# Kernel tuning notes

Hardware: AMD Instinct MI355X
Metric: run time of the kernel (lower is better)

Reference implementation:

```python
import jax, jax.numpy as jnp
import numpy as np

N_A = 50000
N_B = 50000
E = 1600000
D_IN = 128
HID = 128
OUT = 64
NUM_LAYERS = 2


def setup_inputs() -> dict:
    key = jax.random.key(0)
    ks = jax.random.split(key, 16)
    s = 0.05  # weight scale
    return {
        "x_a": jax.random.normal(ks[0], (N_A, D_IN), jnp.float32),
        "x_b": jax.random.normal(ks[1], (N_B, D_IN), jnp.float32),
        "ei_ab": jax.random.randint(ks[2], (2, E), 0, N_A, jnp.int32),  # row0: src in a, row1: dst in b
        "ei_ba": jax.random.randint(ks[3], (2, E), 0, N_B, jnp.int32),
        "Wa_in": jax.random.normal(ks[4], (D_IN, HID), jnp.float32) * s,
        "ba_in": jnp.zeros((HID,), jnp.float32),
        "Wb_in": jax.random.normal(ks[5], (D_IN, HID), jnp.float32) * s,
        "bb_in": jnp.zeros((HID,), jnp.float32),
        "Wl_ab": jax.random.normal(ks[6], (NUM_LAYERS, HID, HID), jnp.float32) * s,
        "Wr_ab": jax.random.normal(ks[7], (NUM_LAYERS, HID, HID), jnp.float32) * s,
        "bl_ab": jnp.zeros((NUM_LAYERS, HID), jnp.float32),
        "Wl_ba": jax.random.normal(ks[8], (NUM_LAYERS, HID, HID), jnp.float32) * s,
        "Wr_ba": jax.random.normal(ks[9], (NUM_LAYERS, HID, HID), jnp.float32) * s,
        "bl_ba": jnp.zeros((NUM_LAYERS, HID), jnp.float32),
        "W_out": jax.random.normal(ks[10], (HID, OUT), jnp.float32) * s,
        "b_out": jnp.zeros((OUT,), jnp.float32),
    }


def _sage_mean(x_src, src_idx, dst_idx, n_dst):
    # mean aggregation of neighbor features onto destination nodes
    msgs = x_src[src_idx]                                   # [E, H] gather
    summed = jax.ops.segment_sum(msgs, dst_idx, num_segments=n_dst)  # [N_dst, H]
    cnt = jax.ops.segment_sum(jnp.ones((src_idx.shape[0],), x_src.dtype), dst_idx, num_segments=n_dst)
    return summed / jnp.maximum(cnt, 1.0)[:, None]


def reference(x_a, x_b, ei_ab, ei_ba, Wa_in, ba_in, Wb_in, bb_in,
              Wl_ab, Wr_ab, bl_ab, Wl_ba, Wr_ba, bl_ba, W_out, b_out):
    # per-node-type input projection + relu
    h_a = jax.nn.relu(x_a @ Wa_in + ba_in)
    h_b = jax.nn.relu(x_b @ Wb_in + bb_in)
    for l in range(NUM_LAYERS):
        # edge type (a -> b): SAGEConv -> new b features
        mean_b = _sage_mean(h_a, ei_ab[0], ei_ab[1], N_B)
        out_b = mean_b @ Wl_ab[l] + bl_ab[l] + h_b @ Wr_ab[l]
        # edge type (b -> a): SAGEConv -> new a features
        mean_a = _sage_mean(h_b, ei_ba[0], ei_ba[1], N_A)
        out_a = mean_a @ Wl_ba[l] + bl_ba[l] + h_a @ Wr_ba[l]
        # HeteroConv aggr='sum': single conv per dst type here; then relu
        h_a = jax.nn.relu(out_a)
        h_b = jax.nn.relu(out_b)
    return h_a @ W_out + b_out
```

## Files before the change

### kernel.cpp

```cpp
#include <hip/hip_runtime.h>

#define N_A   50000
#define N_B   50000
#define NE    1600000
#define HID   128
#define DOUT  64

#define BSH    6
#define BNODES 64
#define NBKT   782
#define ACH    16384

__global__ __launch_bounds__(256)
void bucket_hist(const int* __restrict__ dst, int* __restrict__ cnt, int n) {
    __shared__ int h[NBKT];
    for (int i = threadIdx.x; i < NBKT; i += 256) h[i] = 0;
    __syncthreads();
    for (int i = blockIdx.x * 256 + threadIdx.x; i < n; i += gridDim.x * 256)
        atomicAdd(&h[dst[i] >> BSH], 1);
    __syncthreads();
    for (int i = threadIdx.x; i < NBKT; i += 256)
        if (h[i]) atomicAdd(&cnt[i], h[i]);
}

__global__ __launch_bounds__(1024)
void bucket_scan(const int* __restrict__ cnt, int* __restrict__ base,
                 int* __restrict__ gcur, int etot) {
    __shared__ int s[1024];
    const int g = blockIdx.x;
    cnt  += g * NBKT;
    base += g * (NBKT + 1);
    gcur += g * NBKT;
    int t = threadIdx.x;
    int v = (t < NBKT) ? cnt[t] : 0;
    s[t] = v;
    __syncthreads();
    for (int off = 1; off < 1024; off <<= 1) {
        int x = (t >= off) ? s[t - off] : 0;
        __syncthreads();
        s[t] += x;
        __syncthreads();
    }
    if (t < NBKT) { int b = s[t] - v; base[t] = b; gcur[t] = b; }
    if (t == NBKT) base[t] = etot;
}

__global__ __launch_bounds__(256)
void bucket_scatter(const int* __restrict__ src, const int* __restrict__ dst,
                    int* __restrict__ gcur, unsigned int* __restrict__ ebuf, int n) {
    __shared__ int hist[NBKT];
    __shared__ int lbase[NBKT];
    for (int i = threadIdx.x; i < NBKT; i += 256) hist[i] = 0;
    __syncthreads();
    const int c0 = blockIdx.x * ACH;
    const int c1 = min(c0 + ACH, n);
    for (int i = c0 + threadIdx.x; i < c1; i += 256)
        atomicAdd(&hist[dst[i] >> BSH], 1);
    __syncthreads();
    for (int i = threadIdx.x; i < NBKT; i += 256) {
        int h = hist[i];
        lbase[i] = h ? atomicAdd(&gcur[i], h) : 0;
    }
    __syncthreads();
    for (int i = threadIdx.x; i < NBKT; i += 256) hist[i] = 0;
    __syncthreads();
    for (int i = c0 + threadIdx.x; i < c1; i += 256) {
        int d = dst[i], sv = src[i];
        int b = d >> BSH;
        int p = lbase[b] + atomicAdd(&hist[b], 1);
        ebuf[p] = ((unsigned)(d & (BNODES - 1)) << 16) | (unsigned)sv;
    }
}

__global__ __launch_bounds__(256)
void bucket_csr(const unsigned int* __restrict__ ebuf, const int* __restrict__ base,
                int* __restrict__ indptr, int* __restrict__ col, int nnodes) {
    __shared__ int hist[BNODES];
    __shared__ int lbase[BNODES];
    __shared__ int cur[BNODES];
    const int t = threadIdx.x;
    const int b = blockIdx.x;
    const int e0 = base[b], e1 = base[b + 1];
    if (t < BNODES) { hist[t] = 0; cur[t] = 0; }
    __syncthreads();
    for (int i = e0 + t; i < e1; i += 256)
        atomicAdd(&hist[ebuf[i] >> 16], 1);
    __syncthreads();
    if (t == 0) {
        int acc = 0;
        for (int j = 0; j < BNODES; ++j) { lbase[j] = acc; acc += hist[j]; }
    }
    __syncthreads();
    {
        int node = (b << BSH) + t;
        if (t < BNODES && node <= nnodes) indptr[node] = e0 + lbase[t];
        if (t == BNODES && node - 1 < nnodes && node - 1 == nnodes - 1 && b == NBKT - 1)
            ;
    }
    if (t < BNODES) {
        int node = (b << BSH) + t;
        if (node == nnodes) indptr[node] = e0 + lbase[t];
    }
    if (b == NBKT - 1 && t == 0 && (NBKT << BSH) == nnodes) indptr[nnodes] = e1;
    for (int i = e0 + t; i < e1; i += 256) {
        unsigned pe = ebuf[i];
        int dl = pe >> 16;
        int p = e0 + lbase[dl] + atomicAdd(&cur[dl], 1);
        col[p] = (int)(pe & 0xffffu);
    }
}

__global__ __launch_bounds__(256)
void agg_mean(const float* __restrict__ h, const int* __restrict__ indptr,
              const int* __restrict__ col, float* __restrict__ outm, int n) {
    int w = threadIdx.x >> 6;
    int l = threadIdx.x & 63;
    int v = blockIdx.x * 4 + w;
    if (v >= n) return;
    int s = indptr[v], e = indptr[v + 1];
    const int half = l >> 5;
    const int q    = l & 31;
    const float4* h4 = (const float4*)h;
    float ax = 0.f, ay = 0.f, az = 0.f, aw = 0.f;
    int i = s;
    for (; i + 4 <= e; i += 4) {
        int u0 = col[i + half];
        int u1 = col[i + 2 + half];
        float4 x0 = h4[u0 * 32 + q];
        float4 x1 = h4[u1 * 32 + q];
        ax += x0.x + x1.x; ay += x0.y + x1.y;
        az += x0.z + x1.z; aw += x0.w + x1.w;
    }
    for (; i + 2 <= e; i += 2) {
        int u = col[i + half];
        float4 x = h4[u * 32 + q];
        ax += x.x; ay += x.y; az += x.z; aw += x.w;
    }
    if (i < e && half == 0) {
        float4 x = h4[col[i] * 32 + q];
        ax += x.x; ay += x.y; az += x.z; aw += x.w;
    }
    ax += __shfl_xor(ax, 32);
    ay += __shfl_xor(ay, 32);
    az += __shfl_xor(az, 32);
    aw += __shfl_xor(aw, 32);
    if (half == 0) {
        float inv = 1.0f / fmaxf((float)(e - s), 1.0f);
        float4 o;
        o.x = ax * inv; o.y = ay * inv; o.z = az * inv; o.w = aw * inv;
        ((float4*)outm)[v * 32 + q] = o;
    }
}

#define AS 132

__device__ __forceinline__ void fma4(float4& a, float s, const float4& w) {
    a.x += s * w.x; a.y += s * w.y; a.z += s * w.z; a.w += s * w.w;
}

template <int COLS, bool TWO, bool RELU>
__global__ __launch_bounds__(256)
void gemm_rt(const float* __restrict__ A, const float* __restrict__ B,
             const float* __restrict__ W1, const float* __restrict__ W2,
             const float* __restrict__ bias, float* __restrict__ out, int nrows) {
    constexpr int NCH = COLS / 64;
    __shared__ float Asm[64 * AS];
    __shared__ float Wsm[128 * 64];
    const int t = threadIdx.x;
    const int p = t >> 4, m = t & 15, m4 = m * 4;
    const int r0 = 4 * p;
    const int rbase = blockIdx.x * 64;

    float4 acc[NCH][4];
#pragma unroll
    for (int c = 0; c < NCH; ++c)
#pragma unroll
        for (int i = 0; i < 4; ++i)
            acc[c][i] = make_float4(0.f, 0.f, 0.f, 0.f);

#pragma unroll
    for (int sidx = 0; sidx < (TWO ? 2 : 1); ++sidx) {
        const float* Asrc = (TWO && sidx) ? B : A;
        const float* Wsrc = (TWO && sidx) ? W2 : W1;
        __syncthreads();
        {
            const float4* g = (const float4*)Asrc;
#pragma unroll
            for (int it = 0; it < 8; ++it) {
                int f = t + 256 * it;
                int r = f >> 5, c = f & 31;
                int gr = rbase + r;
                float4 v = make_float4(0.f, 0.f, 0.f, 0.f);
                if (gr < nrows) v = g[(size_t)gr * 32 + c];
                *(float4*)&Asm[r * AS + 4 * c] = v;
            }
        }
#pragma unroll
        for (int ch = 0; ch < NCH; ++ch) {
            if (ch > 0) __syncthreads();
            {
                const float4* gw = (const float4*)Wsrc;
#pragma unroll
                for (int it = 0; it < 8; ++it) {
                    int f = t + 256 * it;
                    int k = f >> 4, c4 = f & 15;
                    float4 v = gw[k * (COLS / 4) + ch * 16 + c4];
                    *(float4*)&Wsm[k * 64 + 4 * c4] = v;
                }
            }
            __syncthreads();
#pragma unroll 2
            for (int k = 0; k < 128; k += 4) {
                float4 w0 = *(const float4*)&Wsm[(k + 0) * 64 + m4];
                float4 w1 = *(const float4*)&Wsm[(k + 1) * 64 + m4];
                float4 w2 = *(const float4*)&Wsm[(k + 2) * 64 + m4];
                float4 w3 = *(const float4*)&Wsm[(k + 3) * 64 + m4];
#pragma unroll
                for (int i = 0; i < 4; ++i) {
                    float4 a = *(const float4*)&Asm[(r0 + i) * AS + k];
                    fma4(acc[ch][i], a.x, w0);
                    fma4(acc[ch][i], a.y, w1);
                    fma4(acc[ch][i], a.z, w2);
                    fma4(acc[ch][i], a.w, w3);
                }
            }
        }
    }

#pragma unroll
    for (int ch = 0; ch < NCH; ++ch) {
        float4 b4 = *(const float4*)&bias[ch * 64 + m4];
#pragma unroll
        for (int i = 0; i < 4; ++i) {
            int r = rbase + r0 + i;
            if (r < nrows) {
                float4 v = acc[ch][i];
                v.x += b4.x; v.y += b4.y; v.z += b4.z; v.w += b4.w;
                if (RELU) {
                    v.x = fmaxf(v.x, 0.f); v.y = fmaxf(v.y, 0.f);
                    v.z = fmaxf(v.z, 0.f); v.w = fmaxf(v.w, 0.f);
                }
                *(float4*)&out[(size_t)r * COLS + ch * 64 + m4] = v;
            }
        }
    }
}

extern "C" void kernel_launch(void* const* d_in, const int* in_sizes, int n_in,
                              void* d_out, int out_size, void* d_ws, size_t ws_size,
                              hipStream_t stream) {
    const float* x_a   = (const float*)d_in[0];
    const float* x_b   = (const float*)d_in[1];
    const int*   ei_ab = (const int*)d_in[2];
    const int*   ei_ba = (const int*)d_in[3];
    const float* Wa_in = (const float*)d_in[4];
    const float* ba_in = (const float*)d_in[5];
    const float* Wb_in = (const float*)d_in[6];
    const float* bb_in = (const float*)d_in[7];
    const float* Wl_ab = (const float*)d_in[8];
    const float* Wr_ab = (const float*)d_in[9];
    const float* bl_ab = (const float*)d_in[10];
    const float* Wl_ba = (const float*)d_in[11];
    const float* Wr_ba = (const float*)d_in[12];
    const float* bl_ba = (const float*)d_in[13];
    const float* W_out = (const float*)d_in[14];
    const float* b_out = (const float*)d_in[15];
    float* out = (float*)d_out;

    char* w = (char*)d_ws;
    auto alloc = [&](size_t bytes) -> void* {
        void* pp = (void*)w;
        w += (bytes + 255) & ~(size_t)255;
        return pp;
    };
    float* hA0 = (float*)alloc((size_t)N_A * HID * 4);
    float* hA1 = (float*)alloc((size_t)N_A * HID * 4);
    float* hB0 = (float*)alloc((size_t)N_B * HID * 4);
    float* hB1 = (float*)alloc((size_t)N_B * HID * 4);
    unsigned int* ebuf_ab = (unsigned int*)alloc((size_t)NE * 4);
    unsigned int* ebuf_ba = (unsigned int*)alloc((size_t)NE * 4);
    int* col_ab   = (int*)alloc((size_t)NE * 4);
    int* col_ba   = (int*)alloc((size_t)NE * 4);
    int* indptr_b = (int*)alloc((size_t)(N_B + 1) * 4);
    int* indptr_a = (int*)alloc((size_t)(N_A + 1) * 4);
    int* cnt  = (int*)alloc((size_t)2 * NBKT * 4);
    int* base = (int*)alloc((size_t)2 * (NBKT + 1) * 4);
    int* gcur = (int*)alloc((size_t)2 * NBKT * 4);

    hipMemsetAsync(cnt, 0, (size_t)2 * NBKT * 4, stream);
    bucket_hist<<<256, 256, 0, stream>>>(ei_ab + NE, cnt, NE);
    bucket_hist<<<256, 256, 0, stream>>>(ei_ba + NE, cnt + NBKT, NE);
    bucket_scan<<<2, 1024, 0, stream>>>(cnt, base, gcur, NE);
    const int scat_blocks = (NE + ACH - 1) / ACH;
    bucket_scatter<<<scat_blocks, 256, 0, stream>>>(ei_ab, ei_ab + NE, gcur, ebuf_ab, NE);
    bucket_scatter<<<scat_blocks, 256, 0, stream>>>(ei_ba, ei_ba + NE, gcur + NBKT, ebuf_ba, NE);
    const int* base_ab = base;
    const int* base_ba = base + (NBKT + 1);
    bucket_csr<<<NBKT, 256, 0, stream>>>(ebuf_ab, base_ab, indptr_b, col_ab, N_B);
    bucket_csr<<<NBKT, 256, 0, stream>>>(ebuf_ba, base_ba, indptr_a, col_ba, N_A);

    const int gemm_blocks_a = (N_A + 63) / 64;
    const int gemm_blocks_b = (N_B + 63) / 64;
    const int agg_blocks_a  = (N_A + 3) / 4;
    const int agg_blocks_b  = (N_B + 3) / 4;

    gemm_rt<128, false, true><<<gemm_blocks_a, 256, 0, stream>>>(
        x_a, nullptr, Wa_in, nullptr, ba_in, hA0, N_A);
    gemm_rt<128, false, true><<<gemm_blocks_b, 256, 0, stream>>>(
        x_b, nullptr, Wb_in, nullptr, bb_in, hB0, N_B);

    float* ha = hA0; float* ha_alt = hA1;
    float* hb = hB0; float* hb_alt = hB1;
    for (int l = 0; l < 2; ++l) {
        const float* wl_ab = Wl_ab + (size_t)l * HID * HID;
        const float* wr_ab = Wr_ab + (size_t)l * HID * HID;
        const float* bias_ab = bl_ab + (size_t)l * HID;
        const float* wl_ba = Wl_ba + (size_t)l * HID * HID;
        const float* wr_ba = Wr_ba + (size_t)l * HID * HID;
        const float* bias_ba = bl_ba + (size_t)l * HID;

        agg_mean<<<agg_blocks_b, 256, 0, stream>>>(ha, indptr_b, col_ab, hb_alt, N_B);
        agg_mean<<<agg_blocks_a, 256, 0, stream>>>(hb, indptr_a, col_ba, ha_alt, N_A);
        gemm_rt<128, true, true><<<gemm_blocks_b, 256, 0, stream>>>(
            hb_alt, hb, wl_ab, wr_ab, bias_ab, hb_alt, N_B);
        gemm_rt<128, true, true><<<gemm_blocks_a, 256, 0, stream>>>(
            ha_alt, ha, wl_ba, wr_ba, bias_ba, ha_alt, N_A);

        float* tmp;
        tmp = ha; ha = ha_alt; ha_alt = tmp;
        tmp = hb; hb = hb_alt; hb_alt = tmp;
    }

    gemm_rt<64, false, false><<<gemm_blocks_a, 256, 0, stream>>>(
        ha, nullptr, W_out, nullptr, b_out, out, N_A);
}
```

Before: 1.012 ms.

## Replace FP32 SIMT GEMMs with split-bf16 MFMA GEMMs and unroll aggregation deeper

Replaces the shared-memory FP32 FMA GEMM with a matrix-core kernel. It uses bf16 MFMA 16x16x32 and a hi/lo bf16 split (three MFMAs per product) to keep near-FP32 accuracy. Weights are pre-split and transposed into bf16 hi/lo buffers by a new prep kernel, and activations are split in registers. The mean aggregation loop is also unrolled to 16 edges per iteration to get more gathers in flight. This adds a prep launch, and the accuracy depends on the three-term split being close enough.

```diff
diff --git a/kernel.cpp b/kernel.cpp
--- a/kernel.cpp
+++ b/kernel.cpp
@@ -10,6 +10,9 @@
 #define BNODES 64
 #define NBKT   782
 #define ACH    16384
+
+typedef __attribute__((ext_vector_type(8))) short bf16x8;
+typedef __attribute__((ext_vector_type(4))) float f32x4;
 
 __global__ __launch_bounds__(256)
 void bucket_hist(const int* __restrict__ dst, int* __restrict__ cnt, int n) {
@@ -91,15 +94,9 @@
         for (int j = 0; j < BNODES; ++j) { lbase[j] = acc; acc += hist[j]; }
     }
     __syncthreads();
-    {
-        int node = (b << BSH) + t;
-        if (t < BNODES && node <= nnodes) indptr[node] = e0 + lbase[t];
-        if (t == BNODES && node - 1 < nnodes && node - 1 == nnodes - 1 && b == NBKT - 1)
-            ;
-    }
     if (t < BNODES) {
         int node = (b << BSH) + t;
-        if (node == nnodes) indptr[node] = e0 + lbase[t];
+        if (node <= nnodes) indptr[node] = e0 + lbase[t];
     }
     if (b == NBKT - 1 && t == 0 && (NBKT << BSH) == nnodes) indptr[nnodes] = e1;
     for (int i = e0 + t; i < e1; i += 256) {
@@ -123,11 +120,23 @@
     const float4* h4 = (const float4*)h;
     float ax = 0.f, ay = 0.f, az = 0.f, aw = 0.f;
     int i = s;
+    for (; i + 16 <= e; i += 16) {
+        int u0 = col[i +  0 + half], u1 = col[i +  2 + half];
+        int u2 = col[i +  4 + half], u3 = col[i +  6 + half];
+        int u4 = col[i +  8 + half], u5 = col[i + 10 + half];
+        int u6 = col[i + 12 + half], u7 = col[i + 14 + half];
+        float4 x0 = h4[u0 * 32 + q], x1 = h4[u1 * 32 + q];
+        float4 x2 = h4[u2 * 32 + q], x3 = h4[u3 * 32 + q];
+        float4 x4 = h4[u4 * 32 + q], x5 = h4[u5 * 32 + q];
+        float4 x6 = h4[u6 * 32 + q], x7 = h4[u7 * 32 + q];
+        ax += (x0.x + x1.x) + (x2.x + x3.x) + (x4.x + x5.x) + (x6.x + x7.x);
+        ay += (x0.y + x1.y) + (x2.y + x3.y) + (x4.y + x5.y) + (x6.y + x7.y);
+        az += (x0.z + x1.z) + (x2.z + x3.z) + (x4.z + x5.z) + (x6.z + x7.z);
+        aw += (x0.w + x1.w) + (x2.w + x3.w) + (x4.w + x5.w) + (x6.w + x7.w);
+    }
     for (; i + 4 <= e; i += 4) {
-        int u0 = col[i + half];
-        int u1 = col[i + 2 + half];
-        float4 x0 = h4[u0 * 32 + q];
-        float4 x1 = h4[u1 * 32 + q];
+        int u0 = col[i + half], u1 = col[i + 2 + half];
+        float4 x0 = h4[u0 * 32 + q], x1 = h4[u1 * 32 + q];
         ax += x0.x + x1.x; ay += x0.y + x1.y;
         az += x0.z + x1.z; aw += x0.w + x1.w;
     }
@@ -152,98 +161,105 @@
     }
 }
 
-#define AS 132
-
-__device__ __forceinline__ void fma4(float4& a, float s, const float4& w) {
-    a.x += s * w.x; a.y += s * w.y; a.z += s * w.z; a.w += s * w.w;
+struct W11 { const float* s[11]; short* dh[11]; short* dl[11]; };
+
+__global__ __launch_bounds__(256)
+void prep_w(W11 P) {
+    int m = blockIdx.y;
+    int ncols = (m == 10) ? DOUT : HID;
+    int e = blockIdx.x * 256 + threadIdx.x;
+    if (e >= HID * ncols) return;
+    int k = e / ncols, n = e - k * ncols;
+    float x = P.s[m][e];
+    unsigned u = __float_as_uint(x);
+    unsigned hb = (u + 0x8000u) & 0xffff0000u;
+    float fl = x - __uint_as_float(hb);
+    P.dh[m][n * HID + k] = (short)(hb >> 16);
+    P.dl[m][n * HID + k] = (short)((__float_as_uint(fl) + 0x8000u) >> 16);
+}
+
+__device__ __forceinline__ void split8(const float4& a0, const float4& a1,
+                                       bf16x8& hi, bf16x8& lo) {
+    float xs[8] = {a0.x, a0.y, a0.z, a0.w, a1.x, a1.y, a1.z, a1.w};
+#pragma unroll
+    for (int j = 0; j < 8; ++j) {
+        unsigned u = __float_as_uint(xs[j]);
+        unsigned hb = (u + 0x8000u) & 0xffff0000u;
+        float fl = xs[j] - __uint_as_float(hb);
+        hi[j] = (short)(hb >> 16);
+        lo[j] = (short)((__float_as_uint(fl) + 0x8000u) >> 16);
+    }
 }
 
 template <int COLS, bool TWO, bool RELU>
 __global__ __launch_bounds__(256)
-void gemm_rt(const float* __restrict__ A, const float* __restrict__ B,
-             const float* __restrict__ W1, const float* __restrict__ W2,
-             const float* __restrict__ bias, float* __restrict__ out, int nrows) {
-    constexpr int NCH = COLS / 64;
-    __shared__ float Asm[64 * AS];
-    __shared__ float Wsm[128 * 64];
-    const int t = threadIdx.x;
-    const int p = t >> 4, m = t & 15, m4 = m * 4;
-    const int r0 = 4 * p;
-    const int rbase = blockIdx.x * 64;
-
-    float4 acc[NCH][4];
-#pragma unroll
-    for (int c = 0; c < NCH; ++c)
-#pragma unroll
-        for (int i = 0; i < 4; ++i)
-            acc[c][i] = make_float4(0.f, 0.f, 0.f, 0.f);
+void gemm_mfma(const float* __restrict__ A, const float* __restrict__ B2,
+               const short* __restrict__ WtH1, const short* __restrict__ WtL1,
+               const short* __restrict__ WtH2, const short* __restrict__ WtL2,
+               const float* __restrict__ bias, float* __restrict__ out, int nrows) {
+    const int wv = threadIdx.x >> 6;
+    if (!TWO && wv * 32 >= COLS) return;
+    const int l = threadIdx.x & 63;
+    const int l16 = l & 15, l4 = l >> 4;
+    const int rbase = blockIdx.x * 32;
+    const int colbase = wv * 32;
+
+    f32x4 acc[2][2] = {};
 
 #pragma unroll
     for (int sidx = 0; sidx < (TWO ? 2 : 1); ++sidx) {
-        const float* Asrc = (TWO && sidx) ? B : A;
-        const float* Wsrc = (TWO && sidx) ? W2 : W1;
-        __syncthreads();
-        {
-            const float4* g = (const float4*)Asrc;
-#pragma unroll
-            for (int it = 0; it < 8; ++it) {
-                int f = t + 256 * it;
-                int r = f >> 5, c = f & 31;
-                int gr = rbase + r;
-                float4 v = make_float4(0.f, 0.f, 0.f, 0.f);
-                if (gr < nrows) v = g[(size_t)gr * 32 + c];
-                *(float4*)&Asm[r * AS + 4 * c] = v;
+        const float* Asrc = (TWO && sidx) ? B2 : A;
+        const short* WH = (TWO && sidx) ? WtH2 : WtH1;
+        const short* WL = (TWO && sidx) ? WtL2 : WtL1;
+#pragma unroll
+        for (int kb = 0; kb < 4; ++kb) {
+            const int k0 = kb * 32 + l4 * 8;
+            bf16x8 bh[2], bl[2];
+#pragma unroll
+            for (int cf = 0; cf < 2; ++cf) {
+                int n = colbase + 16 * cf + l16;
+                bh[cf] = *(const bf16x8*)&WH[n * HID + k0];
+                bl[cf] = *(const bf16x8*)&WL[n * HID + k0];
             }
-        }
-#pragma unroll
-        for (int ch = 0; ch < NCH; ++ch) {
-            if (ch > 0) __syncthreads();
-            {
-                const float4* gw = (const float4*)Wsrc;
-#pragma unroll
-                for (int it = 0; it < 8; ++it) {
-                    int f = t + 256 * it;
-                    int k = f >> 4, c4 = f & 15;
-                    float4 v = gw[k * (COLS / 4) + ch * 16 + c4];
-                    *(float4*)&Wsm[k * 64 + 4 * c4] = v;
+#pragma unroll
+            for (int rf = 0; rf < 2; ++rf) {
+                int r = rbase + 16 * rf + l16;
+                float4 a0 = make_float4(0.f, 0.f, 0.f, 0.f);
+                float4 a1 = make_float4(0.f, 0.f, 0.f, 0.f);
+                if (r < nrows) {
+                    a0 = *(const float4*)&Asrc[(size_t)r * HID + k0];
+                    a1 = *(const float4*)&Asrc[(size_t)r * HID + k0 + 4];
                 }
-            }
-            __syncthreads();
-#pragma unroll 2
-            for (int k = 0; k < 128; k += 4) {
-                float4 w0 = *(const float4*)&Wsm[(k + 0) * 64 + m4];
-                float4 w1 = *(const float4*)&Wsm[(k + 1) * 64 + m4];
-                float4 w2 = *(const float4*)&Wsm[(k + 2) * 64 + m4];
-                float4 w3 = *(const float4*)&Wsm[(k + 3) * 64 + m4];
-#pragma unroll
-                for (int i = 0; i < 4; ++i) {
-                    float4 a = *(const float4*)&Asm[(r0 + i) * AS + k];
-                    fma4(acc[ch][i], a.x, w0);
-                    fma4(acc[ch][i], a.y, w1);
-                    fma4(acc[ch][i], a.z, w2);
-                    fma4(acc[ch][i], a.w, w3);
+                bf16x8 ah, al;
+                split8(a0, a1, ah, al);
+#pragma unroll
+                for (int cf = 0; cf < 2; ++cf) {
+                    acc[rf][cf] = __builtin_amdgcn_mfma_f32_16x16x32_bf16(ah, bh[cf], acc[rf][cf], 0, 0, 0);
+                    acc[rf][cf] = __builtin_amdgcn_mfma_f32_16x16x32_bf16(ah, bl[cf], acc[rf][cf], 0, 0, 0);
+                    acc[rf][cf] = __builtin_amdgcn_mfma_f32_16x16x32_bf16(al, bh[cf], acc[rf][cf], 0, 0, 0);
                 }
             }
         }
     }
 
-#pragma unroll
-    for (int ch = 0; ch < NCH; ++ch) {
-        float4 b4 = *(const float4*)&bias[ch * 64 + m4];
-#pragma unroll
-        for (int i = 0; i < 4; ++i) {
-            int r = rbase + r0 + i;
-            if (r < nrows) {
-                float4 v = acc[ch][i];
-                v.x += b4.x; v.y += b4.y; v.z += b4.z; v.w += b4.w;
-                if (RELU) {
-                    v.x = fmaxf(v.x, 0.f); v.y = fmaxf(v.y, 0.f);
-                    v.z = fmaxf(v.z, 0.f); v.w = fmaxf(v.w, 0.f);
+    if (TWO) __syncthreads();
+
+#pragma unroll
+    for (int rf = 0; rf < 2; ++rf)
+#pragma unroll
+        for (int cf = 0; cf < 2; ++cf) {
+            int colg = colbase + 16 * cf + l16;
+            float bi = bias[colg];
+#pragma unroll
+            for (int r = 0; r < 4; ++r) {
+                int rowg = rbase + 16 * rf + l4 * 4 + r;
+                if (rowg < nrows) {
+                    float vv = acc[rf][cf][r] + bi;
+                    if (RELU) vv = fmaxf(vv, 0.f);
+                    out[(size_t)rowg * COLS + colg] = vv;
                 }
-                *(float4*)&out[(size_t)r * COLS + ch * 64 + m4] = v;
             }
         }
-    }
 }
 
 extern "C" void kernel_launch(void* const* d_in, const int* in_sizes, int n_in,
@@ -286,6 +302,23 @@
     int* cnt  = (int*)alloc((size_t)2 * NBKT * 4);
     int* base = (int*)alloc((size_t)2 * (NBKT + 1) * 4);
     int* gcur = (int*)alloc((size_t)2 * NBKT * 4);
+    short* WtH = (short*)alloc((size_t)(10 * HID * HID + HID * DOUT) * 2);
+    short* WtL = (short*)alloc((size_t)(10 * HID * HID + HID * DOUT) * 2);
+    auto wh = [&](int i) { return WtH + (size_t)i * HID * HID; };
+    auto wl = [&](int i) { return WtL + (size_t)i * HID * HID; };
+
+    {
+        W11 P;
+        const float* srcs[11] = {
+            Wa_in, Wb_in,
+            Wl_ab, Wl_ab + HID * HID,
+            Wr_ab, Wr_ab + HID * HID,
+            Wl_ba, Wl_ba + HID * HID,
+            Wr_ba, Wr_ba + HID * HID,
+            W_out };
+        for (int i = 0; i < 11; ++i) { P.s[i] = srcs[i]; P.dh[i] = wh(i); P.dl[i] = wl(i); }
+        prep_w<<<dim3(64, 11), 256, 0, stream>>>(P);
+    }
 
     hipMemsetAsync(cnt, 0, (size_t)2 * NBKT * 4, stream);
     bucket_hist<<<256, 256, 0, stream>>>(ei_ab + NE, cnt, NE);
@@ -299,38 +332,32 @@
     bucket_csr<<<NBKT, 256, 0, stream>>>(ebuf_ab, base_ab, indptr_b, col_ab, N_B);
     bucket_csr<<<NBKT, 256, 0, stream>>>(ebuf_ba, base_ba, indptr_a, col_ba, N_A);
 
-    const int gemm_blocks_a = (N_A + 63) / 64;
-    const int gemm_blocks_b = (N_B + 63) / 64;
-    const int agg_blocks_a  = (N_A + 3) / 4;
-    const int agg_blocks_b  = (N_B + 3) / 4;
-
-    gemm_rt<128, false, true><<<gemm_blocks_a, 256, 0, stream>>>(
-        x_a, nullptr, Wa_in, nullptr, ba_in, hA0, N_A);
-    gemm_rt<128, false, true><<<gemm_blocks_b, 256, 0, stream>>>(
-        x_b, nullptr, Wb_in, nullptr, bb_in, hB0, N_B);
+    const int gemm_blocks = (N_A + 31) / 32;
+    const int agg_blocks  = (N_A + 3) / 4;
+
+    gemm_mfma<128, false, true><<<gemm_blocks, 256, 0, stream>>>(
+        x_a, nullptr, wh(0), wl(0), nullptr, nullptr, ba_in, hA0, N_A);
+    gemm_mfma<128, false, true><<<gemm_blocks, 256, 0, stream>>>(
+        x_b, nullptr, wh(1), wl(1), nullptr, nullptr, bb_in, hB0, N_B);
 
     float* ha = hA0; float* ha_alt = hA1;
     float* hb = hB0; float* hb_alt = hB1;
     for (int l = 0; l < 2; ++l) {
-        const float* wl_ab = Wl_ab + (size_t)l * HID * HID;
-        const float* wr_ab = Wr_ab + (size_t)l * HID * HID;
         const float* bias_ab = bl_ab + (size_t)l * HID;
-        const float* wl_ba = Wl_ba + (size_t)l * HID * HID;
-        const float* wr_ba = Wr_ba + (size_t)l * HID * HID;
         const float* bias_ba = bl_ba + (size_t)l * HID;
 
-        agg_mean<<<agg_blocks_b, 256, 0, stream>>>(ha, indptr_b, col_ab, hb_alt, N_B);
-        agg_mean<<<agg_blocks_a, 256, 0, stream>>>(hb, indptr_a, col_ba, ha_alt, N_A);
-        gemm_rt<128, true, true><<<gemm_blocks_b, 256, 0, stream>>>(
-            hb_alt, hb, wl_ab, wr_ab, bias_ab, hb_alt, N_B);
-        gemm_rt<128, true, true><<<gemm_blocks_a, 256, 0, stream>>>(
-            ha_alt, ha, wl_ba, wr_ba, bias_ba, ha_alt, N_A);
+        agg_mean<<<agg_blocks, 256, 0, stream>>>(ha, indptr_b, col_ab, hb_alt, N_B);
+        agg_mean<<<agg_blocks, 256, 0, stream>>>(hb, indptr_a, col_ba, ha_alt, N_A);
+        gemm_mfma<128, true, true><<<gemm_blocks, 256, 0, stream>>>(
+            hb_alt, hb, wh(2 + l), wl(2 + l), wh(4 + l), wl(4 + l), bias_ab, hb_alt, N_B);
+        gemm_mfma<128, true, true><<<gemm_blocks, 256, 0, stream>>>(
+            ha_alt, ha, wh(6 + l), wl(6 + l), wh(8 + l), wl(8 + l), bias_ba, ha_alt, N_A);
 
         float* tmp;
         tmp = ha; ha = ha_alt; ha_alt = tmp;
         tmp = hb; hb = hb_alt; hb_alt = tmp;
     }
 
-    gemm_rt<64, false, false><<<gemm_blocks_a, 256, 0, stream>>>(
-        ha, nullptr, W_out, nullptr, b_out, out, N_A);
-}
+    gemm_mfma<64, false, false><<<gemm_blocks, 256, 0, stream>>>(
+        ha, nullptr, wh(10), wl(10), nullptr, nullptr, b_out, out, N_A);
+}
```

Result: no change. 994.6 us (-1.8%).
